# Kernel tuning notes

Measured on AMD Instinct MI355X. Metric: run time of the kernel, lower is better.

Reference implementation:

```python
import jax, jax.numpy as jnp
import numpy as np

KS, S1, S2, TEMP = 7, 4, 1, 10.0
DN = ('NCHW', 'OIHW', 'NCHW')


def _same_pad(h, w, k, stride):
    # Mirrors torch same_padding(): output = ceil(in/stride), asymmetric pad (floor/ceil).
    oh, ow = -(-h // stride), -(-w // stride)
    pr = max(0, (oh - 1) * stride + k - h)
    pc = max(0, (ow - 1) * stride + k - w)
    return ((pr // 2, pr - pr // 2), (pc // 2, pc - pc // 2))


def _unfold(x, k, stride, pad):
    # torch.nn.Unfold: returns [B, C*k*k, nH*nW] with channel-major (c, ki, kj) ordering.
    xp = jnp.pad(x, ((0, 0), (0, 0), pad[0], pad[1]))
    Hp, Wp = xp.shape[2], xp.shape[3]
    nH = (Hp - k) // stride + 1
    nW = (Wp - k) // stride + 1
    rr = stride * jnp.arange(nH)[None, :] + jnp.arange(k)[:, None]  # [k, nH]
    cc = stride * jnp.arange(nW)[None, :] + jnp.arange(k)[:, None]  # [k, nW]
    p = xp[:, :, rr[:, None, :, None], cc[None, :, None, :]]  # [B, C, k, k, nH, nW]
    B, C = x.shape[:2]
    return p.reshape(B, C * k * k, nH * nW)


def _fold(patches, C, k, H, W, pad, stride):
    # torch.nn.functional.fold: scatter-add overlapping patches. patches: [B, L, C*k*k].
    B, L, _ = patches.shape
    nH = (H + 2 * pad - k) // stride + 1
    nW = (W + 2 * pad - k) // stride + 1
    z = patches.reshape(B, nH, nW, C, k, k).transpose(0, 3, 4, 5, 1, 2)  # [B,C,k,k,nH,nW]
    rr = stride * jnp.arange(nH)[None, :] + jnp.arange(k)[:, None]  # [k, nH]
    cc = stride * jnp.arange(nW)[None, :] + jnp.arange(k)[:, None]  # [k, nW]
    out = jnp.zeros((B, C, H + 2 * pad, W + 2 * pad), z.dtype)
    out = out.at[:, :, rr[:, None, :, None], cc[None, :, None, :]].add(z)
    return out[:, :, pad:pad + H, pad:pad + W]


def _conv(x, w, b, s):
    y = jax.lax.conv_general_dilated(x, w, (s, s), 'VALID', dimension_numbers=DN)
    return y + b[None, :, None, None]


def _forward(x, w_theta, b_theta, w_phi0, b_phi0, w_phi1, b_phi1, w_phi2, b_phi2,
             w_g0, b_g0, w_g1, b_g1, w_g2, b_g2, w_out, b_out):
    B, C, H, W = x.shape
    IC = w_theta.shape[0]
    theta = _conv(x, w_theta, b_theta, 1)                      # [B, IC, H, W]
    pad_q = _same_pad(H, W, KS, S1)
    tq = _unfold(theta, KS, S1, pad_q).transpose(0, 2, 1)      # [B, Lq, IC*k*k]
    Lq = tq.shape[1]
    # fold normalization mask (torch uses symmetric padding ksize//2 for the fold path)
    mask = _fold(jnp.ones((1, Lq, KS * KS), x.dtype), 1, KS, H, W, KS // 2, S1)[0, 0]
    phis = ((w_phi0, b_phi0), (w_phi1, b_phi1), (w_phi2, b_phi2))
    gs = ((w_g0, b_g0), (w_g1, b_g1), (w_g2, b_g2))
    outs = []
    for s, (wp, bp), (wg, bg) in zip((1, 2, 4), phis, gs):
        phi = _conv(x, wp, bp, s)                              # [B, IC, H/s, W/s]
        g = _conv(x, wg, bg, s)
        h, w = phi.shape[2], phi.shape[3]
        pad_k = _same_pad(h, w, KS, S2)
        pk = _unfold(phi, KS, S2, pad_k)                       # [B, IC*k*k, Lk]
        gk = _unfold(g, KS, S2, pad_k).transpose(0, 2, 1)      # [B, Lk, IC*k*k]
        score = jnp.einsum('bqc,bck->bqk', tq, pk)             # [B, Lq, Lk]
        attn = jax.nn.softmax(score * TEMP, axis=-1)
        yv = jnp.einsum('bqk,bkc->bqc', attn, gk)              # [B, Lq, IC*k*k]
        outs.append(_fold(yv, IC, KS, H, W, KS // 2, S1) / mask)
    y = jnp.concatenate(outs, axis=1)                          # [B, 3*IC, H, W]
    return _conv(y, w_out, b_out, 1) + x


def setup_inputs() -> dict:
    key = jax.random.key(0)
    ks = jax.random.split(key, 20)
    B, C, H, W, IC = 2, 64, 128, 128, 16
    wscale, bscale = 0.02, 0.01
    d = {'x': jax.random.normal(ks[0], (B, C, H, W), jnp.float32)}
    d['w_theta'] = jax.random.normal(ks[1], (IC, C, 1, 1), jnp.float32) * wscale
    d['b_theta'] = jax.random.normal(ks[2], (IC,), jnp.float32) * bscale
    for i, s in enumerate((1, 2, 4)):
        d[f'w_phi{i}'] = jax.random.normal(ks[3 + 4 * i], (IC, C, s, s), jnp.float32) * wscale
        d[f'b_phi{i}'] = jax.random.normal(ks[4 + 4 * i], (IC,), jnp.float32) * bscale
        d[f'w_g{i}'] = jax.random.normal(ks[5 + 4 * i], (IC, C, s, s), jnp.float32) * wscale
        d[f'b_g{i}'] = jax.random.normal(ks[6 + 4 * i], (IC,), jnp.float32) * bscale
    d['w_out'] = jax.random.normal(ks[15], (C, 3 * IC, 1, 1), jnp.float32) * wscale
    d['b_out'] = jax.random.normal(ks[16], (C,), jnp.float32) * bscale
    return d


def reference(x, w_theta, b_theta, w_phi0, b_phi0, w_phi1, b_phi1, w_phi2, b_phi2,
              w_g0, b_g0, w_g1, b_g1, w_g2, b_g2, w_out, b_out):
    return _forward(x, w_theta, b_theta, w_phi0, b_phi0, w_phi1, b_phi1, w_phi2, b_phi2,
                    w_g0, b_g0, w_g1, b_g1, w_g2, b_g2, w_out, b_out)
```

## Files before the change

kernel.cpp:

```cpp
#include <hip/hip_runtime.h>
#include <stdint.h>

typedef __attribute__((ext_vector_type(8))) short bf16x8;
typedef __attribute__((ext_vector_type(4))) float f32x4;
typedef __attribute__((ext_vector_type(4))) unsigned int u32x4;

#define DEV __device__ __forceinline__

DEV float bf2f(unsigned short u){ union{unsigned int i; float f;} v; v.i=((unsigned int)u)<<16; return v.f; }
DEV unsigned short f2bf(float f){ union{float f; unsigned int i;} v; v.f=f; unsigned int x=v.i;
  return (unsigned short)((x + 0x7fffu + ((x>>16)&1u)) >> 16); }

__global__ void k_zero(uint4* __restrict__ p, int n16)
{
  int idx = blockIdx.x*256 + threadIdx.x;
  if (idx < n16) p[idx] = uint4{0,0,0,0};
}

DEV void prep1_body(int bid, const float* __restrict__ x,
                    const float* __restrict__ wt, const float* __restrict__ bt,
                    const float* __restrict__ wp, const float* __restrict__ bp,
                    const float* __restrict__ wg, const float* __restrict__ bg,
                    unsigned short* __restrict__ th, unsigned short* __restrict__ ph,
                    float* __restrict__ gt, char* smemc)
{
  float (*red)[64][48] = (float(*)[64][48])smemc;
  float* wl = (float*)(smemc + 36864);
  int tid = threadIdx.x;
  for (int u = tid; u < 768; u += 256) {
    float4 v;
    if (u < 256) v = ((const float4*)wt)[u];
    else if (u < 512) v = ((const float4*)wp)[u-256];
    else v = ((const float4*)wg)[u-512];
    ((float4*)wl)[u] = v;
  }
  __syncthreads();
  int grp = tid >> 6, pixl = tid & 63;
  int pix = bid*64 + pixl;
  int b = pix >> 14, p = pix & 16383, i = p >> 7, j = p & 127;
  float a[48];
#pragma unroll
  for (int c=0;c<48;++c) a[c]=0.f;
  const float* xb = x + (size_t)b*64*16384 + p;
#pragma unroll
  for (int c4=0; c4<4; ++c4) {
    int cc = grp*16 + c4*4;
    float xv[4];
#pragma unroll
    for (int u=0;u<4;++u) xv[u] = xb[(size_t)(cc+u)*16384];
#pragma unroll
    for (int ic=0;ic<16;++ic) {
      float4 w0 = *(const float4*)(wl + ic*64 + cc);
      float4 w1 = *(const float4*)(wl + 1024 + ic*64 + cc);
      float4 w2 = *(const float4*)(wl + 2048 + ic*64 + cc);
      a[ic]    += xv[0]*w0.x + xv[1]*w0.y + xv[2]*w0.z + xv[3]*w0.w;
      a[16+ic] += xv[0]*w1.x + xv[1]*w1.y + xv[2]*w1.z + xv[3]*w1.w;
      a[32+ic] += xv[0]*w2.x + xv[1]*w2.y + xv[2]*w2.z + xv[3]*w2.w;
    }
  }
  if (grp) {
#pragma unroll
    for (int c=0;c<48;++c) red[grp-1][pixl][c] = a[c];
  }
  __syncthreads();
  if (grp == 0) {
#pragma unroll
    for (int c=0;c<48;++c) a[c] += red[0][pixl][c] + red[1][pixl][c] + red[2][pixl][c];
    const float TEMPC = 14.426950408889634f;
    unsigned short o[16];
#pragma unroll
    for (int ic=0;ic<16;++ic) o[ic] = f2bf((a[ic]+bt[ic])*TEMPC);
    uint4* d0 = (uint4*)(th + ((size_t)(b*134 + i+3)*136 + (j+3))*16);
    d0[0]=*(uint4*)&o[0]; d0[1]=*(uint4*)&o[8];
#pragma unroll
    for (int ic=0;ic<16;++ic) o[ic] = f2bf(a[16+ic]+bp[ic]);
    uint4* d1 = (uint4*)(ph + ((size_t)(b*134 + i+3)*136 + (j+3))*16);
    d1[0]=*(uint4*)&o[0]; d1[1]=*(uint4*)&o[8];
#pragma unroll
    for (int ic=0;ic<16;++ic)
      gt[(((size_t)b*16+ic)*134 + i+3)*136 + (j+3)] = a[32+ic]+bg[ic];
  }
}

DEV void conv2_body(int bid, const float* __restrict__ x,
                    const float* __restrict__ wp, const float* __restrict__ bp,
                    const float* __restrict__ wg, const float* __restrict__ bg,
                    unsigned short* __restrict__ phi, float* __restrict__ gt, char* smemc)
{
  float (*red)[64][32] = (float(*)[64][32])smemc;
  float* wl = (float*)(smemc + 24576);
  int tid = threadIdx.x;
  for (int u = tid; u < 2048; u += 256) {
    float4 v = (u < 1024) ? ((const float4*)wp)[u] : ((const float4*)wg)[u-1024];
    ((float4*)wl)[u] = v;
  }
  __syncthreads();
  int grp = tid >> 6, pixl = tid & 63;
  int pix = bid*64 + pixl;
  int b = pix >> 12, p = pix & 4095, i = p >> 6, j = p & 63;
  float a[32];
#pragma unroll
  for (int c=0;c<32;++c) a[c]=0.f;
  const float* xb = x + (size_t)b*64*16384 + (i*2)*128 + j*2;
#pragma unroll
  for (int c0=0; c0<16; ++c0) {
    int cc = grp*16 + c0;
    const float* xp = xb + (size_t)cc*16384;
    float xv[4];
    xv[0]=xp[0]; xv[1]=xp[1]; xv[2]=xp[128]; xv[3]=xp[129];
#pragma unroll
    for (int ic=0;ic<16;++ic) {
      float4 w0 = *(const float4*)(wl + (ic*64+cc)*4);
      float4 w1 = *(const float4*)(wl + 4096 + (ic*64+cc)*4);
      a[ic]    += xv[0]*w0.x + xv[1]*w0.y + xv[2]*w0.z + xv[3]*w0.w;
      a[16+ic] += xv[0]*w1.x + xv[1]*w1.y + xv[2]*w1.z + xv[3]*w1.w;
    }
  }
  if (grp) {
#pragma unroll
    for (int c=0;c<32;++c) red[grp-1][pixl][c] = a[c];
  }
  __syncthreads();
  if (grp == 0) {
#pragma unroll
    for (int c=0;c<32;++c) a[c] += red[0][pixl][c] + red[1][pixl][c] + red[2][pixl][c];
    unsigned short o[16];
#pragma unroll
    for (int ic=0;ic<16;++ic) o[ic] = f2bf(a[ic]+bp[ic]);
    uint4* d1 = (uint4*)(phi + ((size_t)(b*70 + i+3)*72 + (j+3))*16);
    d1[0]=*(uint4*)&o[0]; d1[1]=*(uint4*)&o[8];
#pragma unroll
    for (int ic=0;ic<16;++ic)
      gt[(((size_t)b*16+ic)*70 + i+3)*72 + (j+3)] = a[16+ic]+bg[ic];
  }
}

DEV void conv4_body(int bid, const float* __restrict__ x,
                    const float* __restrict__ wp, const float* __restrict__ wg,
                    const float* __restrict__ bp, const float* __restrict__ bg,
                    unsigned short* __restrict__ phi, float* __restrict__ gt, char* smemc)
{
  float (*xs)[1028] = (float(*)[1028])smemc;
  int tid = threadIdx.x;
  int pix0 = bid*8;
  for (int idx = tid; idx < 8*1024; idx += 256) {
    int pl = idx >> 10, e = idx & 1023;
    int pix = pix0 + pl; int b = pix >> 10, p = pix & 1023, i = p >> 5, j = p & 31;
    int cc = e >> 4, a_ = (e >> 2) & 3, bb = e & 3;
    xs[pl][e] = x[(((size_t)b*64+cc)*128 + i*4+a_)*128 + j*4+bb];
  }
  __syncthreads();
  int pp = tid >> 5, icp = tid & 31;
  int pix = pix0 + pp; int b = pix >> 10, p = pix & 1023, i = p >> 5, j = p & 31;
  int ic = icp & 15;
  const float* wsrc = ((icp < 16) ? wp : wg) + ic*1024;
  float acc = 0.f;
#pragma unroll 8
  for (int k4=0; k4<256; ++k4) {
    float4 xv = *(const float4*)(&xs[pp][k4*4]);
    float4 wv = *(const float4*)(wsrc + k4*4);
    acc += xv.x*wv.x + xv.y*wv.y + xv.z*wv.z + xv.w*wv.w;
  }
  if (icp < 16)
    phi[(((size_t)(b*38 + i+3)*40) + (j+3))*16 + ic] = f2bf(acc + bp[ic]);
  else
    gt[(((size_t)b*16+ic)*38 + i+3)*40 + (j+3)] = acc + bg[ic];
}

__global__ void k_prep_all(const float* __restrict__ x,
                           const float* __restrict__ wt, const float* __restrict__ bt,
                           const float* __restrict__ wp0, const float* __restrict__ bp0,
                           const float* __restrict__ wg0, const float* __restrict__ bg0,
                           const float* __restrict__ wp1, const float* __restrict__ bp1,
                           const float* __restrict__ wg1, const float* __restrict__ bg1,
                           const float* __restrict__ wp2, const float* __restrict__ wg2,
                           const float* __restrict__ bp2, const float* __restrict__ bg2,
                           unsigned short* __restrict__ th, unsigned short* __restrict__ ph0,
                           float* __restrict__ gt0,
                           unsigned short* __restrict__ ph1, float* __restrict__ gt1,
                           unsigned short* __restrict__ ph2, float* __restrict__ gt2)
{
  __shared__ __align__(16) char smem[57344];
  int bid = blockIdx.x;
  if (bid < 512)      prep1_body(bid, x, wt,bt, wp0,bp0, wg0,bg0, th, ph0, gt0, smem);
  else if (bid < 640) conv2_body(bid-512, x, wp1,bp1, wg1,bg1, ph1, gt1, smem);
  else                conv4_body(bid-640, x, wp2,wg2, bp2, bg2, ph2, gt2, smem);
}

template<int HP, int WX, int HS>
DEV void shift_body(int idx, const float* __restrict__ gt, unsigned short* __restrict__ g8b)
{
  const int XB = HS/32;
  int xkg = idx & 3;
  int c = (idx >> 2) & 15;
  int t = idx >> 6;
  int xb = t % XB; t /= XB;
  int y = t % HP; t /= HP;
  int sh = t & 7; int b = t >> 3;
  const float* src = gt + (((size_t)b*16+c)*HP + y)*WX + xb*32 + xkg*8 + sh;
  unsigned short o[8];
#pragma unroll
  for (int j=0;j<8;++j) o[j] = f2bf(src[j]);
  unsigned short* dst = g8b + ((((size_t)(b*8+sh)*HP + y)*XB + xb)*16 + c)*32 + xkg*8;
  *(uint4*)dst = *(uint4*)&o[0];
}

__global__ void k_shift_all(const float* __restrict__ gt0, const float* __restrict__ gt1,
                            const float* __restrict__ gt2,
                            unsigned short* __restrict__ g80, unsigned short* __restrict__ g81,
                            unsigned short* __restrict__ g82)
{
  const int T0 = 2*8*134*4*16*4;
  const int T1 = 2*8*70*2*16*4;
  const int T2 = 2*8*38*1*16*4;
  int idx = blockIdx.x*256 + threadIdx.x;
  if (idx < T0) { shift_body<134,136,128>(idx, gt0, g80); return; }
  idx -= T0;
  if (idx < T1) { shift_body<70,72,64>(idx, gt1, g81); return; }
  idx -= T1;
  if (idx < T2) { shift_body<38,40,32>(idx, gt2, g82); }
}

template<int HS, int LG, int HP, int WX, int CK, int NCH>
DEV void attn_body(int bid, int slot0,
                   const unsigned short* __restrict__ th,
                   const unsigned short* __restrict__ phi,
                   const unsigned short* __restrict__ g8b,
                   unsigned short* __restrict__ accP, float* __restrict__ lP, char* smem)
{
  const int PO = 30464;
  int tid = threadIdx.x;
  int w = tid >> 6, lane = tid & 63, l15 = lane & 15, g = lane >> 4;
  int chunk, b, qt;
  if (NCH == 8) { chunk = bid & 7; b = (bid >> 3) & 1; qt = bid >> 4; }
  else          { chunk = bid & 3; b = (bid >> 2) & 1; qt = bid >> 3; }
  int q0 = qt * 32;
  int slot = slot0 + chunk;

  const char* thB  = (const char*)th  + (size_t)b*134*136*32;
  const char* phiB = (const char*)phi + (size_t)b*HP*WX*32;

  for (int u = tid; u < 7*136*2; u += 512) {
    int half = u & 1; int cu = (u >> 1) % 136; int r = (u >> 1) / 136;
    uint4 v = *(const uint4*)(thB + (((4*qt+2+r)*136 + cu)*32 + half*16));
    int la = (((r*136 + cu)*32) + half*16) ^ (((cu >> 2) & 7) << 4);
    *(uint4*)(smem + la) = v;
  }
  __syncthreads();

  f32x4 acc[2][7];
#pragma unroll
  for (int rt=0;rt<2;++rt)
#pragma unroll
    for (int et=0;et<7;++et) acc[rt][et] = f32x4{0.f,0.f,0.f,0.f};
  float lacc[2][4];
#pragma unroll
  for (int rt=0;rt<2;++rt)
#pragma unroll
    for (int r=0;r<4;++r) lacc[rt][r] = 0.f;

  const int XBv = HS/32;
  const char* g8B  = (const char*)g8b + (size_t)b*8*HP*XBv*1024;
  const int EPL = HP*XBv*1024;
  int laneVb = l15*64 + g*16;
  int xrP = (l15 & 7) << 4;
  int colb = 4*l15 + 2;
  int hb = (g & 1) << 4;
  const bf16x8 ZV = {0,0,0,0,0,0,0,0};
  const int ITERS = CK/256;
  const float SHIFT = 64.0f, CLAMP = 120.0f;

  auto QK = [&](int it) {
    int k0 = chunk*CK + it*256;
    int po = PO + ((it & 1) << 14);
    f32x4 sc[2][2];
#pragma unroll
    for (int rt=0;rt<2;++rt){ sc[rt][0]=f32x4{0.f,0.f,0.f,0.f}; sc[rt][1]=f32x4{0.f,0.f,0.f,0.f}; }
    int kr_w = (k0 + w*32) >> LG;
    int kc_w = (w*32) & (HS-1);
    int base0 = (kr_w*WX + kc_w + l15)*32 + hb;
    int base1 = base0 + 512;
#pragma unroll
    for (int ks=0; ks<25; ++ks) {
      int p0 = 2*ks;
      int p1 = (2*ks+1 > 48) ? 48 : 2*ks+1;
      int dr0 = p0/7, dc0 = p0%7;
      int dr1 = p1/7, dc1 = p1%7;
      int c0 = colb + dc0, c1 = colb + dc1;
      int la0 = ((dr0*136 + c0)*32 + hb) ^ (((c0 >> 2) & 7) << 4);
      int la1 = ((dr1*136 + c1)*32 + hb) ^ (((c1 >> 2) & 7) << 4);
      int laA = (g & 2) ? la1 : la0;
      int KB0 = (dr0*WX + dc0)*32;
      int KB1 = (dr1*WX + dc1)*32;
      int selB = (g & 2) ? KB1 : KB0;
      bf16x8 a0 = *(const bf16x8*)(smem + laA);
      bf16x8 a1 = *(const bf16x8*)(smem + laA + 2048);
      if (ks == 24) {
        bool z = (g & 2) != 0;
        a0 = z ? ZV : a0; a1 = z ? ZV : a1;
      }
      bf16x8 b0 = *(const bf16x8*)(phiB + base0 + selB);
      bf16x8 b1 = *(const bf16x8*)(phiB + base1 + selB);
      sc[0][0] = __builtin_amdgcn_mfma_f32_16x16x32_bf16(a0, b0, sc[0][0], 0,0,0);
      sc[0][1] = __builtin_amdgcn_mfma_f32_16x16x32_bf16(a0, b1, sc[0][1], 0,0,0);
      sc[1][0] = __builtin_amdgcn_mfma_f32_16x16x32_bf16(a1, b0, sc[1][0], 0,0,0);
      sc[1][1] = __builtin_amdgcn_mfma_f32_16x16x32_bf16(a1, b1, sc[1][1], 0,0,0);
    }
#pragma unroll
    for (int rt=0;rt<2;++rt) {
#pragma unroll
      for (int r=0;r<4;++r) {
        float pa = __builtin_amdgcn_exp2f(fminf(sc[rt][0][r] - SHIFT, CLAMP));
        float pb = __builtin_amdgcn_exp2f(fminf(sc[rt][1][r] - SHIFT, CLAMP));
        lacc[rt][r] += pa + pb;
        int q_ = rt*16 + g*4 + r;
        int offa = q_*512 + (w*32 + l15)*2;      offa ^= (q_&7)<<4;
        int offb = q_*512 + (w*32 + 16 + l15)*2; offb ^= (q_&7)<<4;
        *(unsigned short*)(smem + po + offa) = f2bf(pa);
        *(unsigned short*)(smem + po + offb) = f2bf(pb);
      }
    }
  };

  auto PV = [&](int it) {
    if (w >= 7) return;
    int k0 = chunk*CK + it*256;
    int po = PO + ((it & 1) << 14);
#pragma unroll
    for (int ks2=0; ks2<8; ++ks2) {
      int kk = k0 + ks2*32;
      int krv = kk >> LG;
      int kcb = kk & (HS-1);
      bf16x8 pf[2];
#pragma unroll
      for (int rt=0;rt<2;++rt) {
        int off = (rt*16 + l15)*512 + ks2*64 + g*16;
        off ^= xrP;
        pf[rt] = *(const bf16x8*)(smem + po + off);
      }
      int vb = ((krv + w)*XBv + (kcb >> 5))*1024 + laneVb;
      bf16x8 vf[7];
#pragma unroll
      for (int et=0;et<7;++et) {
        u32x4 t0 = __builtin_nontemporal_load((const u32x4*)(g8B + vb + et*EPL));
        vf[et] = *(bf16x8*)&t0;
      }
      __builtin_amdgcn_s_setprio(1);
#pragma unroll
      for (int rt=0;rt<2;++rt)
#pragma unroll
        for (int et=0;et<7;++et)
          acc[rt][et] = __builtin_amdgcn_mfma_f32_16x16x32_bf16(pf[rt], vf[et], acc[rt][et], 0,0,0);
      __builtin_amdgcn_s_setprio(0);
    }
  };

  QK(0);
  __syncthreads();
#pragma unroll 1
  for (int it = 1; it < ITERS; ++it) {
    PV(it-1);
    QK(it);
    __syncthreads();
  }
  PV(ITERS-1);

  if (w < 7) {
    unsigned short* accB = accP +
      ((((size_t)(slot*2 + b)*32 + qt)*7 + w)*14)*256;
#pragma unroll
    for (int rt=0;rt<2;++rt)
#pragma unroll
      for (int et=0;et<7;++et)
#pragma unroll
        for (int r=0;r<4;++r)
          __builtin_nontemporal_store(f2bf(acc[rt][et][r]),
            &accB[(size_t)(rt*7 + et)*256 + r*64 + lane]);
  }
#pragma unroll
  for (int st=1; st<16; st<<=1)
#pragma unroll
    for (int rt=0;rt<2;++rt)
#pragma unroll
      for (int r=0;r<4;++r) lacc[rt][r] += __shfl_xor(lacc[rt][r], st);
  if (l15 == 0) {
#pragma unroll
    for (int rt=0;rt<2;++rt)
#pragma unroll
      for (int r=0;r<4;++r)
        lP[((size_t)((slot*2 + b)*8 + w) << 10) + q0 + rt*16 + g*4 + r] = lacc[rt][r];
  }
}

__global__ void __launch_bounds__(512, 2)
k_attn_all(const unsigned short* __restrict__ th,
           const unsigned short* __restrict__ ph0, const unsigned short* __restrict__ ph1,
           const unsigned short* __restrict__ ph2,
           const unsigned short* __restrict__ g80, const unsigned short* __restrict__ g81,
           const unsigned short* __restrict__ g82,
           unsigned short* __restrict__ accP, float* __restrict__ lP)
{
  __shared__ __align__(16) char smem[30464 + 2*16384];
  int bid = blockIdx.x;
  if (bid < 512)       attn_body<128,7,134,136,2048,8>(bid,      0,  th, ph0, g80, accP, lP, smem);
  else if (bid < 1024) attn_body<64,6,70,72,512,8>   (bid-512,  8,  th, ph1, g81, accP, lP, smem);
  else                 attn_body<32,5,38,40,256,4>   (bid-1024, 16, th, ph2, g82, accP, lP, smem);
}

__global__ void k_comb1_all(const float* __restrict__ lP, float* __restrict__ lG)
{
  int idx = blockIdx.x*256 + threadIdx.x;
  if (idx >= 3*2048) return;
  int sc = idx >> 11, i2 = idx & 2047;
  int b = i2 >> 10, q = i2 & 1023;
  const int NCH[3] = {8,8,4}, S0[3] = {0,8,16};
  float l = 0.f;
  for (int c=0;c<NCH[sc];++c)
#pragma unroll
    for (int w=0;w<8;++w)
      l += lP[((size_t)(((S0[sc]+c)*2 + b)*8 + w) << 10) + q];
  lG[idx] = l;
}

__global__ void k_comb2_all(const unsigned short* __restrict__ accP,
                            const float* __restrict__ lG, float* __restrict__ yvfP)
{
  int t8 = blockIdx.x*256 + threadIdx.x;
  if (t8 >= 3*200704) return;
  int sc = t8 / 200704;
  int rem = t8 - sc*200704;
  int e = rem*8;
  int low = e & 255;
  int r = low >> 6, g = (low >> 4) & 3;
  int tile = e >> 8;
  int et = tile % 7; int tt = tile / 7;
  int rt = tt & 1; tt >>= 1;
  int w = tt % 7; tt /= 7;
  int qt = tt & 31; int b = tt >> 5;
  int bq = (b << 10) + qt*32 + rt*16 + g*4 + r;
  const int NCH[3] = {8,8,4}, S0[3] = {0,8,16};
  float s[8];
#pragma unroll
  for (int u=0;u<8;++u) s[u]=0.f;
  for (int ch=0; ch<NCH[sc]; ++ch) {
    const unsigned short* ap = accP + (size_t)(S0[sc]+ch)*1605632 + e;
    u32x4 v = __builtin_nontemporal_load((const u32x4*)ap);
    const unsigned short* pv = (const unsigned short*)&v;
#pragma unroll
    for (int u=0;u<8;++u) s[u] += bf2f(pv[u]);
  }
  float inv = 1.0f / lG[sc*2048 + bq];
  float* dst = yvfP + (size_t)sc*1605632 + e;
  float4 o0, o1;
  o0.x=s[0]*inv; o0.y=s[1]*inv; o0.z=s[2]*inv; o0.w=s[3]*inv;
  o1.x=s[4]*inv; o1.y=s[5]*inv; o1.z=s[6]*inv; o1.w=s[7]*inv;
  *(float4*)dst = o0; *(float4*)(dst+4) = o1;
}

__global__ void k_foldfinal(const float* __restrict__ yvfP, const float* __restrict__ wo,
                            const float* __restrict__ bo, const float* __restrict__ x,
                            float* __restrict__ out)
{
  __shared__ float wl[32*48];
  int half = blockIdx.x >> 7;
  int pixb = blockIdx.x & 127;
  for (int t = threadIdx.x; t < 32*48; t += 256) wl[t] = wo[half*32*48 + t];
  __syncthreads();
  int idx = pixb*256 + threadIdx.x;
  int j = idx & 127; int t = idx >> 7; int i = t & 127; int b = t >> 7;

  int drs[2], qis[2], cnti=0;
  int dcs[2], qjs[2], cntj=0;
#pragma unroll
  for (int dr=0; dr<7; ++dr) {
    int tr = i + 3 - dr;
    if (tr >= 0 && (tr & 3) == 0 && (tr >> 2) < 32) { drs[cnti]=dr; qis[cnti]=tr>>2; ++cnti; }
  }
#pragma unroll
  for (int dc=0; dc<7; ++dc) {
    int tc = j + 3 - dc;
    if (tc >= 0 && (tc & 3) == 0 && (tc >> 2) < 32) { dcs[cntj]=dc; qjs[cntj]=tc>>2; ++cntj; }
  }
  float inv = 1.0f / (float)(cnti*cntj);

  float y[48];
#pragma unroll
  for (int sc=0; sc<3; ++sc) {
    const float* yb = yvfP + (size_t)sc*1605632;
    float a[16];
#pragma unroll
    for (int c=0;c<16;++c) a[c]=0.f;
    for (int u=0; u<cnti; ++u) {
      for (int v=0; v<cntj; ++v) {
        int q = qis[u]*32 + qjs[v];
        int qt = q >> 5, rt = (q >> 4) & 1, gg = (q >> 2) & 3, rr = q & 3;
        int off = ((((b*32 + qt)*7 + drs[u])*2 + rt)*7 + dcs[v])*256 + rr*64 + gg*16;
        const float* src = yb + off;
        float4 v0 = *(const float4*)(src);
        float4 v1 = *(const float4*)(src+4);
        float4 v2 = *(const float4*)(src+8);
        float4 v3 = *(const float4*)(src+12);
        a[0]+=v0.x; a[1]+=v0.y; a[2]+=v0.z; a[3]+=v0.w;
        a[4]+=v1.x; a[5]+=v1.y; a[6]+=v1.z; a[7]+=v1.w;
        a[8]+=v2.x; a[9]+=v2.y; a[10]+=v2.z; a[11]+=v2.w;
        a[12]+=v3.x; a[13]+=v3.y; a[14]+=v3.z; a[15]+=v3.w;
      }
    }
#pragma unroll
    for (int c=0;c<16;++c) y[sc*16+c] = a[c]*inv;
  }

  const float* xb = x + (size_t)b*64*16384 + i*128 + j;
  float* ob = out + (size_t)b*64*16384 + i*128 + j;
  for (int o=0;o<32;++o) {
    int oc = half*32 + o;
    float s = bo[oc];
#pragma unroll
    for (int c=0;c<48;++c) s += y[c]*wl[o*48+c];
    ob[(size_t)oc*16384] = s + xb[(size_t)oc*16384];
  }
}

extern "C" void kernel_launch(void* const* d_in, const int* in_sizes, int n_in,
                              void* d_out, int out_size, void* d_ws, size_t ws_size,
                              hipStream_t stream)
{
  const float* x  = (const float*)d_in[0];
  const float* wt = (const float*)d_in[1];
  const float* bt = (const float*)d_in[2];
  const float* wp0= (const float*)d_in[3];
  const float* bp0= (const float*)d_in[4];
  const float* wg0= (const float*)d_in[5];
  const float* bg0= (const float*)d_in[6];
  const float* wp1= (const float*)d_in[7];
  const float* bp1= (const float*)d_in[8];
  const float* wg1= (const float*)d_in[9];
  const float* bg1= (const float*)d_in[10];
  const float* wp2= (const float*)d_in[11];
  const float* bp2= (const float*)d_in[12];
  const float* wg2= (const float*)d_in[13];
  const float* bg2= (const float*)d_in[14];
  const float* wo = (const float*)d_in[15];
  const float* bo = (const float*)d_in[16];
  float* out = (float*)d_out;
  (void)in_sizes; (void)n_in; (void)out_size; (void)ws_size;

  char* ws = (char*)d_ws;
  size_t off = 0;
  auto alloc = [&](size_t bytes)->char* { char* p = ws + off; off += (bytes + 255) & ~(size_t)255; return p; };
  unsigned short* th  = (unsigned short*)alloc(2ull*134*136*16*2);
  unsigned short* ph0 = (unsigned short*)alloc(2ull*134*136*16*2);
  unsigned short* ph1 = (unsigned short*)alloc(2ull*70*72*16*2);
  unsigned short* ph2 = (unsigned short*)alloc(2ull*38*40*16*2);
  float* gt0 = (float*)alloc(2ull*16*134*136*4);
  float* gt1 = (float*)alloc(2ull*16*70*72*4);
  float* gt2 = (float*)alloc(2ull*16*38*40*4);
  size_t zeroBytes = off;
  unsigned short* g80 = (unsigned short*)alloc(2ull*8*134*4*512*2);
  unsigned short* g81 = (unsigned short*)alloc(2ull*8*70*2*512*2);
  unsigned short* g82 = (unsigned short*)alloc(2ull*8*38*1*512*2);
  float* lP  = (float*)alloc(20ull*2*8*1024*4);
  float* lG  = (float*)alloc(3ull*2048*4);
  unsigned short* accP = (unsigned short*)alloc(20ull*2048*784*2);
  float* yvfP = (float*)alloc(3ull*2048*784*4);

  int n16 = (int)(zeroBytes/16);
  k_zero<<<(n16+255)/256,256,0,stream>>>((uint4*)ws, n16);
  k_prep_all<<<896,256,0,stream>>>(x, wt,bt, wp0,bp0,wg0,bg0, wp1,bp1,wg1,bg1,
                                   wp2,wg2, bp2,bg2, th,ph0,gt0, ph1,gt1, ph2,gt2);
  k_shift_all<<<(548864+143360+38912+255)/256,256,0,stream>>>(gt0,gt1,gt2, g80,g81,g82);
  k_attn_all<<<1280,512,0,stream>>>(th, ph0,ph1,ph2, g80,g81,g82, accP, lP);
  k_comb1_all<<<(3*2048+255)/256,256,0,stream>>>(lP, lG);
  k_comb2_all<<<(3*200704+255)/256,256,0,stream>>>(accP, lG, yvfP);
  k_foldfinal<<<256,256,0,stream>>>(yvfP, wo, bo, x, out);
}
```

Before: 412.4 us.

## Stage scale-0 phi rows into an LDS ring buffer via global_load_lds

```diff
diff --git a/kernel.cpp b/kernel.cpp
--- a/kernel.cpp
+++ b/kernel.cpp
@@ -221,14 +221,16 @@
   if (idx < T2) { shift_body<38,40,32>(idx, gt2, g82); }
 }
 
-template<int HS, int LG, int HP, int WX, int CK, int NCH>
+template<int HS, int LG, int HP, int WX, int CK, int NCH, bool RING>
 DEV void attn_body(int bid, int slot0,
                    const unsigned short* __restrict__ th,
                    const unsigned short* __restrict__ phi,
                    const unsigned short* __restrict__ g8b,
                    unsigned short* __restrict__ accP, float* __restrict__ lP, char* smem)
 {
-  const int PO = 30464;
+  const int PO   = 30464;
+  const int PHI0 = 30464;
+  const int PO_R = 65280;
   int tid = threadIdx.x;
   int w = tid >> 6, lane = tid & 63, l15 = lane & 15, g = lane >> 4;
   int chunk, b, qt;
@@ -270,16 +272,26 @@
   const int ITERS = CK/256;
   const float SHIFT = 64.0f, CLAMP = 120.0f;
 
+  auto stage_row = [&](int row) {
+    int slotr = row & 7;
+    const char* src = phiB + (size_t)row*WX*32;
+    int w2 = tid >> 6;
+    char* dstb = smem + PHI0 + slotr*4352 + w2*1024;
+    if (tid < 272)
+      __builtin_amdgcn_global_load_lds(
+        (const __attribute__((address_space(1))) unsigned int*)(src + tid*16),
+        (__attribute__((address_space(3))) unsigned int*)dstb, 16, 0, 0);
+  };
+
   auto QK = [&](int it) {
     int k0 = chunk*CK + it*256;
-    int po = PO + ((it & 1) << 14);
+    int po = RING ? PO_R : (PO + ((it & 1) << 14));
     f32x4 sc[2][2];
 #pragma unroll
     for (int rt=0;rt<2;++rt){ sc[rt][0]=f32x4{0.f,0.f,0.f,0.f}; sc[rt][1]=f32x4{0.f,0.f,0.f,0.f}; }
     int kr_w = (k0 + w*32) >> LG;
     int kc_w = (w*32) & (HS-1);
     int base0 = (kr_w*WX + kc_w + l15)*32 + hb;
-    int base1 = base0 + 512;
 #pragma unroll
     for (int ks=0; ks<25; ++ks) {
       int p0 = 2*ks;
@@ -290,17 +302,26 @@
       int la0 = ((dr0*136 + c0)*32 + hb) ^ (((c0 >> 2) & 7) << 4);
       int la1 = ((dr1*136 + c1)*32 + hb) ^ (((c1 >> 2) & 7) << 4);
       int laA = (g & 2) ? la1 : la0;
-      int KB0 = (dr0*WX + dc0)*32;
-      int KB1 = (dr1*WX + dc1)*32;
-      int selB = (g & 2) ? KB1 : KB0;
       bf16x8 a0 = *(const bf16x8*)(smem + laA);
       bf16x8 a1 = *(const bf16x8*)(smem + laA + 2048);
       if (ks == 24) {
         bool z = (g & 2) != 0;
         a0 = z ? ZV : a0; a1 = z ? ZV : a1;
       }
-      bf16x8 b0 = *(const bf16x8*)(phiB + base0 + selB);
-      bf16x8 b1 = *(const bf16x8*)(phiB + base1 + selB);
+      bf16x8 b0, b1;
+      if constexpr (RING) {
+        int laB0 = ((kr_w + dr0) & 7)*4352 + (kc_w + l15 + dc0)*32 + hb;
+        int laB1 = ((kr_w + dr1) & 7)*4352 + (kc_w + l15 + dc1)*32 + hb;
+        int laB = (g & 2) ? laB1 : laB0;
+        b0 = *(const bf16x8*)(smem + PHI0 + laB);
+        b1 = *(const bf16x8*)(smem + PHI0 + laB + 512);
+      } else {
+        int KB0 = (dr0*WX + dc0)*32;
+        int KB1 = (dr1*WX + dc1)*32;
+        int selB = (g & 2) ? KB1 : KB0;
+        b0 = *(const bf16x8*)(phiB + base0 + selB);
+        b1 = *(const bf16x8*)(phiB + base0 + 512 + selB);
+      }
       sc[0][0] = __builtin_amdgcn_mfma_f32_16x16x32_bf16(a0, b0, sc[0][0], 0,0,0);
       sc[0][1] = __builtin_amdgcn_mfma_f32_16x16x32_bf16(a0, b1, sc[0][1], 0,0,0);
       sc[1][0] = __builtin_amdgcn_mfma_f32_16x16x32_bf16(a1, b0, sc[1][0], 0,0,0);
@@ -325,7 +346,7 @@
   auto PV = [&](int it) {
     if (w >= 7) return;
     int k0 = chunk*CK + it*256;
-    int po = PO + ((it & 1) << 14);
+    int po = RING ? PO_R : (PO + ((it & 1) << 14));
 #pragma unroll
     for (int ks2=0; ks2<8; ++ks2) {
       int kk = k0 + ks2*32;
@@ -355,15 +376,34 @@
     }
   };
 
-  QK(0);
-  __syncthreads();
+  if constexpr (RING) {
+    int r0 = (chunk*CK) >> LG;
+#pragma unroll
+    for (int rr = 0; rr < 8; ++rr) stage_row(r0 + rr);
+    __syncthreads();
 #pragma unroll 1
-  for (int it = 1; it < ITERS; ++it) {
-    PV(it-1);
-    QK(it);
+    for (int it = 0; it < ITERS; ++it) {
+      QK(it);
+      __syncthreads();
+      if (it+1 < ITERS) {
+        int nr = ((chunk*CK + (it+1)*256) >> LG) + 6;
+        stage_row(nr);
+        stage_row(nr+1);
+      }
+      PV(it);
+      __syncthreads();
+    }
+  } else {
+    QK(0);
     __syncthreads();
-  }
-  PV(ITERS-1);
+#pragma unroll 1
+    for (int it = 1; it < ITERS; ++it) {
+      PV(it-1);
+      QK(it);
+      __syncthreads();
+    }
+    PV(ITERS-1);
+  }
 
   if (w < 7) {
     unsigned short* accB = accP +
@@ -400,11 +440,11 @@
            const unsigned short* __restrict__ g82,
            unsigned short* __restrict__ accP, float* __restrict__ lP)
 {
-  __shared__ __align__(16) char smem[30464 + 2*16384];
+  __shared__ __align__(16) char smem[81664];
   int bid = blockIdx.x;
-  if (bid < 512)       attn_body<128,7,134,136,2048,8>(bid,      0,  th, ph0, g80, accP, lP, smem);
-  else if (bid < 1024) attn_body<64,6,70,72,512,8>   (bid-512,  8,  th, ph1, g81, accP, lP, smem);
-  else                 attn_body<32,5,38,40,256,4>   (bid-1024, 16, th, ph2, g82, accP, lP, smem);
+  if (bid < 512)       attn_body<128,7,134,136,2048,8,true> (bid,      0,  th, ph0, g80, accP, lP, smem);
+  else if (bid < 1024) attn_body<64,6,70,72,512,8,false>    (bid-512,  8,  th, ph1, g81, accP, lP, smem);
+  else                 attn_body<32,5,38,40,256,4,false>    (bid-1024, 16, th, ph2, g82, accP, lP, smem);
 }
 
 __global__ void k_comb1_all(const float* __restrict__ lP, float* __restrict__ lG)
```

Result: faster. 386.9 us (-6.2%).
